# Kernel tuning notes

Hardware: AMD Instinct MI355X
Metric: run time of the kernel (lower is better)

Reference implementation:

```python
import jax, jax.numpy as jnp
import numpy as np

H = 4    # heads
DK = 5   # d_k = d_model // h = 20 // 4
D = 20   # d_model


def _proj(x, W, b):
    # x: [B,S,D] -> [B,H,S,DK]
    B, S, _ = x.shape
    y = x @ W.T + b
    return y.reshape(B, S, H, DK).transpose(0, 2, 1, 3)


def _attn(q, k, v, mask4):
    # q,k,v: [B,H,S,DK]; mask4: [B,1,1,S]
    scores = jnp.einsum('bhqd,bhkd->bhqk', q, k) / jnp.sqrt(jnp.asarray(DK, q.dtype))
    scores = jnp.where(mask4 == 0, jnp.asarray(-1e9, q.dtype), scores)
    p = jax.nn.softmax(scores, axis=-1)  # dropout omitted (eval mode)
    return jnp.einsum('bhqk,bhkd->bhqd', p, v)


def setup_inputs() -> dict:
    key = jax.random.key(0)
    ks = jax.random.split(key, 12)
    B, S = 8, 2048
    scale = 1.0 / np.sqrt(D)
    inp = {
        'query': jax.random.normal(ks[0], (B, S, D), dtype=jnp.float32),
        'key': jax.random.normal(ks[1], (B, S, D), dtype=jnp.float32),
        'value': jax.random.normal(ks[2], (B, S, D), dtype=jnp.float32),
        'mask': jax.random.randint(ks[3], (B, S), 0, 2, dtype=jnp.int32),
    }
    for i in range(4):
        inp[f'W{i}'] = jax.random.normal(ks[4 + 2 * i], (D, D), dtype=jnp.float32) * scale
        inp[f'b{i}'] = jax.random.normal(ks[5 + 2 * i], (D,), dtype=jnp.float32) * 0.01
    return inp


def reference(query, key, value, mask, W0, b0, W1, b1, W2, b2, W3, b3):
    B, S, _ = query.shape
    mask4 = mask[:, None, None, :]  # [B,1,1,S]
    # Six permuted (arg-to-linear0, arg-to-linear1, arg-to-linear2) variants,
    # exactly as the torch forward: (q,k,k),(k,q,q),(q,v,v),(v,q,q),(k,v,v),(v,k,k)
    triples = [
        (query, key, key), (key, query, query),
        (query, value, value), (value, query, query),
        (key, value, value), (value, key, key),
    ]
    out = None
    for a, bb, c in triples:
        o = _attn(_proj(a, W0, b0), _proj(bb, W1, b1), _proj(c, W2, b2), mask4)
        out = o if out is None else out + o
    # merge heads: [B,H,S,DK] -> [B,S,D]
    out = out.transpose(0, 2, 1, 3).reshape(B, S, H * DK)
    return out @ W3.T + b3
```

## Files before the change

kernel.cpp:

```cpp
#include <hip/hip_runtime.h>
#include <cstdint>
#include <cstddef>

#define B    8
#define SEQ  2048
#define H    4
#define DKN  5
#define DIM  20
#define PRE8 8
#define SENTB ((short)0xC2FC)
#define ONEB  ((short)0x3F80)
#define B128  ((short)0x4300)
#define PBIASM 12599162.0f

typedef short short8 __attribute__((ext_vector_type(8)));
typedef float f32x16 __attribute__((ext_vector_type(16)));

static __device__ __forceinline__ unsigned short bf16b(float x) {
    union { float f; unsigned u; } v; v.f = x;
    unsigned r = v.u + 0x7FFFu + ((v.u >> 16) & 1u);
    return (unsigned short)(r >> 16);
}
static __device__ __forceinline__ float bf16f(unsigned short h) {
    union { unsigned u; float f; } v; v.u = ((unsigned)h) << 16;
    return v.f;
}
static __device__ __forceinline__ unsigned pk_pbits(float ta, float tb) {
    unsigned ia, ib;
    __builtin_memcpy(&ia, &ta, 4);
    __builtin_memcpy(&ib, &tb, 4);
    return __builtin_amdgcn_perm(ib, ia, 0x05040100u);
}
static __device__ __forceinline__ int sig32(int t) {
    return (t & 19) | ((t & 4) << 1) | ((t & 8) >> 1);
}


__global__ __launch_bounds__(256) void proj_kernel(
    const float* __restrict__ q, const float* __restrict__ k, const float* __restrict__ v,
    const float* __restrict__ W0, const float* __restrict__ b0,
    const float* __restrict__ W1, const float* __restrict__ b1,
    const float* __restrict__ W2, const float* __restrict__ b2,
    const int* __restrict__ mask,
    short* __restrict__ Qt, short* __restrict__ Kt, short* __restrict__ Vt,
    int* __restrict__ meta)
{
    __shared__ float Ws[3][DIM * DIM];
    __shared__ float bsh[3][DIM];
    __shared__ int   widx[256];
    __shared__ int   cntS;

    int tid = threadIdx.x;
    int blk = blockIdx.x;
    int w   = blk & 7;  blk >>= 3;
    int h   = blk & 3;  blk >>= 2;
    int bb  = blk & 7;  blk >>= 3;
    int x   = blk;
    int s0  = w * 256;

    for (int i = tid; i < DIM * DIM; i += 256) {
        Ws[0][i] = W0[i]; Ws[1][i] = W1[i]; Ws[2][i] = W2[i];
    }
    if (tid < DIM) { bsh[0][tid] = b0[tid]; bsh[1][tid] = b1[tid]; bsh[2][tid] = b2[tid]; }

    if (tid < 64) {
        const int* mrow = mask + bb * SEQ;
        int base = 0;
        for (int ch = 0; ch < SEQ; ch += 64) {
            int mv = mrow[ch + tid];
            unsigned long long bal = __ballot(mv != 0);
            int pos = base + (int)__popcll(bal & ((1ull << tid) - 1ull));
            if (mv && pos >= s0 && pos < s0 + 256) widx[pos - s0] = ch + tid;
            base += (int)__popcll(bal);
        }
        if (tid == 0) {
            cntS = base;
            if (x == 0 && h == 0 && w == 0) meta[bb] = base;
        }
    }
    __syncthreads();

    int  cnt   = cntS;
    int  c     = s0 + tid;
    bool valid = c < cnt;
    int  gs    = valid ? widx[tid] : 0;

    const float QSC = 0.44721359549995793f * 1.4426950408889634f * 128.0f;
    const float* base = (x == 0) ? q : ((x == 1) ? k : v);

    float xq[DIM], xg[DIM];
    {
        const float4* r4 = (const float4*)(base + (size_t)(bb * SEQ + c) * DIM);
        const float4* g4 = (const float4*)(base + (size_t)(bb * SEQ + gs) * DIM);
        #pragma unroll
        for (int i = 0; i < 5; ++i) {
            float4 a = r4[i], g = g4[i];
            xq[i*4+0]=a.x; xq[i*4+1]=a.y; xq[i*4+2]=a.z; xq[i*4+3]=a.w;
            xg[i*4+0]=g.x; xg[i*4+1]=g.y; xg[i*4+2]=g.z; xg[i*4+3]=g.w;
        }
    }

    #define DOT20(xv, t, j, dst) {                                        \
        float acc_ = bsh[t][j];                                           \
        const float4* wr_ = (const float4*)&Ws[t][(j) * DIM];             \
        _Pragma("unroll")                                                 \
        for (int i4 = 0; i4 < 5; ++i4) {                                  \
            float4 w_ = wr_[i4];                                          \
            acc_ += (xv)[i4*4+0]*w_.x + (xv)[i4*4+1]*w_.y                 \
                  + (xv)[i4*4+2]*w_.z + (xv)[i4*4+3]*w_.w;                \
        }                                                                 \
        dst = acc_;                                                       \
    }

    size_t row = ((size_t)(x * B + bb) * H + h) * SEQ + c;

    short8 qhi = {0, 0, 0, 0, 0, B128, 0, 0};
    short8 qlo = {0, 0, 0, 0, 0, 0, 0, 0};
    #pragma unroll
    for (int d = 0; d < DKN; ++d) {
        float y; DOT20(xq, 0, h * DKN + d, y);
        y *= QSC;
        unsigned short hb = bf16b(y);
        qhi[d] = (short)hb;
        qlo[d] = (short)bf16b(y - bf16f(hb));
    }
    ((short8*)Qt)[row * 2 + 0] = qhi;
    ((short8*)Qt)[row * 2 + 1] = qlo;

    short8 rk = {0, 0, 0, 0, 0, valid ? (short)0 : SENTB, 0, 0};
    if (valid) {
        #pragma unroll
        for (int d = 0; d < DKN; ++d) {
            float y; DOT20(xg, 1, h * DKN + d, y);
            rk[d] = (short)bf16b(y);
        }
    }
    ((short8*)Kt)[row] = rk;

    if (valid) {
        size_t vb = ((size_t)(x * B + bb) * H + h) * 8 * SEQ;
        size_t vcell = vb + (size_t)(c >> 5) * 256 + sig32(c & 31);
        #pragma unroll
        for (int d = 0; d < DKN; ++d) {
            float y; DOT20(xg, 2, h * DKN + d, y);
            Vt[vcell + (size_t)d * 32] = (short)bf16b(y);
        }
        Vt[vcell + (size_t)5 * 32] = ONEB;
    }
}

__global__ __launch_bounds__(128, 4) void attn_kernel(
    const short* __restrict__ Qt, const short* __restrict__ Kt,
    const short* __restrict__ Vt, const int* __restrict__ meta,
    float* __restrict__ pre)
{
    int lane = threadIdx.x & 63;
    int l31  = lane & 31, half = lane >> 5;

    int wid  = blockIdx.x;
    int qtq  = wid / 192;
    int grp  = wid - qtq * 192;
    int h    = grp & 3;  grp >>= 2;
    int b    = grp & 7;  grp >>= 3;
    int p    = grp;
    int a    = (0x212010 >> (4 * p)) & 0xF;
    int kv   = (0x120201 >> (4 * p)) & 0xF;
    int qt0  = qtq * 4 + (threadIdx.x >> 6) * 2;

    int cnt  = meta[b];
    int kend = (cnt + 63) & ~63;

    const short*  Qb = Qt + ((size_t)(a  * B + b) * H + h) * SEQ * 16;
    const short8* Kb = (const short8*)Kt + ((size_t)(kv * B + b) * H + h) * SEQ;
    const short*  Vb = Vt + ((size_t)(kv * B + b) * H + h) * 8 * SEQ;
    const short*  Vr = Vb + (size_t)(l31 & 7) * 32 + half * 8;

    short8 qf[2];
    f32x16 acc[2];
    f32x16 zc = {0.f,0.f,0.f,0.f,0.f,0.f,0.f,0.f,0.f,0.f,0.f,0.f,0.f,0.f,0.f,0.f};
    f32x16 sb = {PBIASM,PBIASM,PBIASM,PBIASM,PBIASM,PBIASM,PBIASM,PBIASM,
                 PBIASM,PBIASM,PBIASM,PBIASM,PBIASM,PBIASM,PBIASM,PBIASM};
    #pragma unroll
    for (int t = 0; t < 2; ++t) {
        int qb = (qt0 + t) * 32;
        qf[t]  = *(const short8*)(Qb + (size_t)(qb + l31) * 16 + half * 8);
        acc[t] = zc;
    }

    short8 kfA = Kb[l31],      kfB = Kb[32 + l31];
    short8 vaA = *(const short8*)(Vr);
    short8 vcA = *(const short8*)(Vr + 16);
    short8 vaB = *(const short8*)(Vr + 256);
    short8 vcB = *(const short8*)(Vr + 272);

    for (int c0 = 0; c0 < kend; c0 += 64) {
        int c1 = c0 + 64;
        const short* Vn = Vr + (size_t)c1 * 8;

        short8 kfA_n = Kb[c1 + l31];
        short8 vaA_n = *(const short8*)(Vn);
        short8 vcA_n = *(const short8*)(Vn + 16);

        __builtin_amdgcn_s_setprio(1);
        #pragma unroll
        for (int t = 0; t < 2; ++t) {
            f32x16 dA = __builtin_amdgcn_mfma_f32_32x32x16_bf16(kfA, qf[t], sb, 0, 0, 0);
            unsigned p0[4], p1[4];
            #pragma unroll
            for (int r = 0; r < 4; ++r) {
                p0[r] = pk_pbits(dA[2 * r],     dA[2 * r + 1]);
                p1[r] = pk_pbits(dA[2 * r + 8], dA[2 * r + 9]);
            }
            short8 f0, f1;
            __builtin_memcpy(&f0, p0, 16);
            __builtin_memcpy(&f1, p1, 16);
            acc[t] = __builtin_amdgcn_mfma_f32_32x32x16_bf16(vaA, f0, acc[t], 0, 0, 0);
            acc[t] = __builtin_amdgcn_mfma_f32_32x32x16_bf16(vcA, f1, acc[t], 0, 0, 0);
        }
        __builtin_amdgcn_s_setprio(0);
        kfA = kfA_n; vaA = vaA_n; vcA = vcA_n;

        short8 kfB_n = Kb[c1 + 32 + l31];
        short8 vaB_n = *(const short8*)(Vn + 256);
        short8 vcB_n = *(const short8*)(Vn + 272);

        __builtin_amdgcn_s_setprio(1);
        #pragma unroll
        for (int t = 0; t < 2; ++t) {
            f32x16 dB = __builtin_amdgcn_mfma_f32_32x32x16_bf16(kfB, qf[t], sb, 0, 0, 0);
            unsigned p0[4], p1[4];
            #pragma unroll
            for (int r = 0; r < 4; ++r) {
                p0[r] = pk_pbits(dB[2 * r],     dB[2 * r + 1]);
                p1[r] = pk_pbits(dB[2 * r + 8], dB[2 * r + 9]);
            }
            short8 f0, f1;
            __builtin_memcpy(&f0, p0, 16);
            __builtin_memcpy(&f1, p1, 16);
            acc[t] = __builtin_amdgcn_mfma_f32_32x32x16_bf16(vaB, f0, acc[t], 0, 0, 0);
            acc[t] = __builtin_amdgcn_mfma_f32_32x32x16_bf16(vcB, f1, acc[t], 0, 0, 0);
        }
        __builtin_amdgcn_s_setprio(0);
        kfB = kfB_n; vaB = vaB_n; vcB = vcB_n;
    }

    float* base0 = pre + (((size_t)p * B + b) * H + h) * SEQ * PRE8;
    #pragma unroll
    for (int t = 0; t < 2; ++t) {
        int qb = (qt0 + t) * 32;
        float lv  = __shfl(acc[t][1], 32 + l31, 64);
        float inv = 1.0f / lv;
        float* dst = base0 + (size_t)(qb + l31) * PRE8;
        if (half == 0)
            *(float4*)dst = make_float4(acc[t][0]*inv, acc[t][1]*inv,
                                        acc[t][2]*inv, acc[t][3]*inv);
        else
            dst[4] = acc[t][0] * inv;
    }
}

__global__ __launch_bounds__(64) void final_kernel(
    const float* __restrict__ pre,
    const float* __restrict__ W3, const float* __restrict__ b3,
    float* __restrict__ out)
{
    __shared__ float Ws[DIM * DIM];
    __shared__ float bs[DIM];
    int tid = threadIdx.x;
    for (int i = tid; i < DIM * DIM; i += 64) Ws[i] = W3[i];
    if (tid < DIM) bs[tid] = b3[tid];
    __syncthreads();

    int g = blockIdx.x * 64 + tid;
    int b = g / SEQ;
    int s = g - b * SEQ;

    float x[DIM];
    #pragma unroll
    for (int i = 0; i < DIM; ++i) x[i] = 0.f;

    for (int p = 0; p < 6; ++p) {
        #pragma unroll
        for (int h = 0; h < H; ++h) {
            const float* sr = pre + (((size_t)p * B + b) * H + h) * SEQ * PRE8
                                  + (size_t)s * PRE8;
            float4 a = *(const float4*)sr;
            float  a4 = sr[4];
            x[h * DKN + 0] += a.x; x[h * DKN + 1] += a.y; x[h * DKN + 2] += a.z;
            x[h * DKN + 3] += a.w; x[h * DKN + 4] += a4;
        }
    }

    float y[DIM];
    for (int j = 0; j < DIM; ++j) {
        float acc = bs[j];
        const float4* wr = (const float4*)&Ws[j * DIM];
        #pragma unroll
        for (int i4 = 0; i4 < 5; ++i4) {
            float4 w = wr[i4];
            acc += x[i4*4+0]*w.x + x[i4*4+1]*w.y + x[i4*4+2]*w.z + x[i4*4+3]*w.w;
        }
        y[j] = acc;
    }
    float4* dst = (float4*)(out + (size_t)(b * SEQ + s) * DIM);
    #pragma unroll
    for (int j4 = 0; j4 < 5; ++j4)
        dst[j4] = make_float4(y[j4*4+0], y[j4*4+1], y[j4*4+2], y[j4*4+3]);
}

extern "C" void kernel_launch(void* const* d_in, const int* in_sizes, int n_in,
                              void* d_out, int out_size, void* d_ws, size_t ws_size,
                              hipStream_t stream) {
    const float* q    = (const float*)d_in[0];
    const float* k    = (const float*)d_in[1];
    const float* v    = (const float*)d_in[2];
    const int*   mask = (const int*)d_in[3];
    const float* W0 = (const float*)d_in[4];  const float* b0 = (const float*)d_in[5];
    const float* W1 = (const float*)d_in[6];  const float* b1 = (const float*)d_in[7];
    const float* W2 = (const float*)d_in[8];  const float* b2 = (const float*)d_in[9];
    const float* W3 = (const float*)d_in[10]; const float* b3 = (const float*)d_in[11];

    const size_t NROW = (size_t)3 * B * H * SEQ;
    short* Qt = (short*)d_ws;
    short* Kt = Qt + NROW * 16;
    short* Vt = Kt + NROW * 8;
    float* pre = (float*)(Vt + NROW * 8);
    int*   meta = (int*)(pre + (size_t)6 * B * H * SEQ * PRE8);
    float* out = (float*)d_out;

    proj_kernel<<<dim3(3 * B * H * (SEQ / 256)), dim3(256), 0, stream>>>(
        q, k, v, W0, b0, W1, b1, W2, b2, mask, Qt, Kt, Vt, meta);
    attn_kernel<<<dim3(6 * B * H * 16), dim3(128), 0, stream>>>(
        Qt, Kt, Vt, meta, pre);
    final_kernel<<<dim3(B * SEQ / 64), dim3(64), 0, stream>>>(pre, W3, b3, out);
}
```

Baseline: 144.0 us.

## Stage K/V tiles through LDS via async global_load_lds double buffering

Replaces direct register prefetch of K and V fragments from global memory with asynchronous global-to-LDS copies into a per-wave double buffer. Fragments are then read from LDS, with an explicit vmcnt wait ensuring the current buffer has landed while the next one loads. The aim is to cut VGPR pressure and make global loads wide and coalesced, at the cost of extra LDS traffic, LDS reads on the critical path and reliance on correct wait counts. There is no workgroup barrier because each wave uses its own buffer.

```diff
diff --git a/kernel.cpp b/kernel.cpp
--- a/kernel.cpp
+++ b/kernel.cpp
@@ -33,6 +33,12 @@
 }
 static __device__ __forceinline__ int sig32(int t) {
     return (t & 19) | ((t & 4) << 1) | ((t & 8) >> 1);
+}
+
+typedef unsigned __attribute__((address_space(1))) gas_u32;
+typedef unsigned __attribute__((address_space(3))) las_u32;
+static __device__ __forceinline__ void glds16(const void* g, void* l) {
+    __builtin_amdgcn_global_load_lds((const gas_u32*)g, (las_u32*)l, 16, 0, 0);
 }
 
 
@@ -154,6 +160,9 @@
     const short* __restrict__ Vt, const int* __restrict__ meta,
     float* __restrict__ pre)
 {
+    __shared__ char lds[2][2][2048];
+
+    int wv   = threadIdx.x >> 6;
     int lane = threadIdx.x & 63;
     int l31  = lane & 31, half = lane >> 5;
 
@@ -165,15 +174,18 @@
     int p    = grp;
     int a    = (0x212010 >> (4 * p)) & 0xF;
     int kv   = (0x120201 >> (4 * p)) & 0xF;
-    int qt0  = qtq * 4 + (threadIdx.x >> 6) * 2;
+    int qt0  = qtq * 4 + wv * 2;
 
     int cnt  = meta[b];
     int kend = (cnt + 63) & ~63;
 
-    const short*  Qb = Qt + ((size_t)(a  * B + b) * H + h) * SEQ * 16;
-    const short8* Kb = (const short8*)Kt + ((size_t)(kv * B + b) * H + h) * SEQ;
-    const short*  Vb = Vt + ((size_t)(kv * B + b) * H + h) * 8 * SEQ;
-    const short*  Vr = Vb + (size_t)(l31 & 7) * 32 + half * 8;
+    const short* Qb  = Qt + ((size_t)(a  * B + b) * H + h) * SEQ * 16;
+    const char*  Kst = (const char*)(Kt + ((size_t)(kv * B + b) * H + h) * SEQ * 8);
+    const char*  Vst = (const char*)(Vt + ((size_t)(kv * B + b) * H + h) * 8 * SEQ);
+
+    char* myl = &lds[wv][0][0];
+    int koff = l31 * 16;
+    int voff = 1024 + (l31 & 7) * 64 + half * 16;
 
     short8 qf[2];
     f32x16 acc[2];
@@ -187,61 +199,60 @@
         acc[t] = zc;
     }
 
-    short8 kfA = Kb[l31],      kfB = Kb[32 + l31];
-    short8 vaA = *(const short8*)(Vr);
-    short8 vcA = *(const short8*)(Vr + 16);
-    short8 vaB = *(const short8*)(Vr + 256);
-    short8 vcB = *(const short8*)(Vr + 272);
-
+    glds16(Kst + lane * 16, myl);
+    glds16(Vst + lane * 16, myl + 1024);
+
+    #define PVSTEP(D, VA, VC, ACC) {                                          \
+        unsigned p0_[4], p1_[4];                                              \
+        _Pragma("unroll")                                                     \
+        for (int r = 0; r < 4; ++r) {                                         \
+            p0_[r] = pk_pbits(D[2 * r],     D[2 * r + 1]);                    \
+            p1_[r] = pk_pbits(D[2 * r + 8], D[2 * r + 9]);                    \
+        }                                                                     \
+        short8 f0_, f1_;                                                      \
+        __builtin_memcpy(&f0_, p0_, 16);                                      \
+        __builtin_memcpy(&f1_, p1_, 16);                                      \
+        ACC = __builtin_amdgcn_mfma_f32_32x32x16_bf16(VA, f0_, ACC, 0, 0, 0); \
+        ACC = __builtin_amdgcn_mfma_f32_32x32x16_bf16(VC, f1_, ACC, 0, 0, 0); \
+    }
+
+    int buf = 0;
     for (int c0 = 0; c0 < kend; c0 += 64) {
-        int c1 = c0 + 64;
-        const short* Vn = Vr + (size_t)c1 * 8;
-
-        short8 kfA_n = Kb[c1 + l31];
-        short8 vaA_n = *(const short8*)(Vn);
-        short8 vcA_n = *(const short8*)(Vn + 16);
+        size_t c1b = (size_t)(c0 + 64) * 16;
+        char* nb = myl + ((buf ^ 1) << 11);
+        glds16(Kst + c1b + lane * 16, nb);
+        glds16(Vst + c1b + lane * 16, nb + 1024);
+
+        __builtin_amdgcn_sched_barrier(0);
+        asm volatile("s_waitcnt vmcnt(2)" ::: "memory");
+        __builtin_amdgcn_sched_barrier(0);
+
+        const char* cb = myl + (buf << 11);
+        short8 kfA = *(const short8*)(cb + koff);
+        short8 vaA = *(const short8*)(cb + voff);
+        short8 vcA = *(const short8*)(cb + voff + 32);
 
         __builtin_amdgcn_s_setprio(1);
         #pragma unroll
         for (int t = 0; t < 2; ++t) {
             f32x16 dA = __builtin_amdgcn_mfma_f32_32x32x16_bf16(kfA, qf[t], sb, 0, 0, 0);
-            unsigned p0[4], p1[4];
-            #pragma unroll
-            for (int r = 0; r < 4; ++r) {
-                p0[r] = pk_pbits(dA[2 * r],     dA[2 * r + 1]);
-                p1[r] = pk_pbits(dA[2 * r + 8], dA[2 * r + 9]);
-            }
-            short8 f0, f1;
-            __builtin_memcpy(&f0, p0, 16);
-            __builtin_memcpy(&f1, p1, 16);
-            acc[t] = __builtin_amdgcn_mfma_f32_32x32x16_bf16(vaA, f0, acc[t], 0, 0, 0);
-            acc[t] = __builtin_amdgcn_mfma_f32_32x32x16_bf16(vcA, f1, acc[t], 0, 0, 0);
+            PVSTEP(dA, vaA, vcA, acc[t]);
         }
         __builtin_amdgcn_s_setprio(0);
-        kfA = kfA_n; vaA = vaA_n; vcA = vcA_n;
-
-        short8 kfB_n = Kb[c1 + 32 + l31];
-        short8 vaB_n = *(const short8*)(Vn + 256);
-        short8 vcB_n = *(const short8*)(Vn + 272);
+
+        short8 kfB = *(const short8*)(cb + koff + 512);
+        short8 vaB = *(const short8*)(cb + voff + 512);
+        short8 vcB = *(const short8*)(cb + voff + 544);
 
         __builtin_amdgcn_s_setprio(1);
         #pragma unroll
         for (int t = 0; t < 2; ++t) {
             f32x16 dB = __builtin_amdgcn_mfma_f32_32x32x16_bf16(kfB, qf[t], sb, 0, 0, 0);
-            unsigned p0[4], p1[4];
-            #pragma unroll
-            for (int r = 0; r < 4; ++r) {
-                p0[r] = pk_pbits(dB[2 * r],     dB[2 * r + 1]);
-                p1[r] = pk_pbits(dB[2 * r + 8], dB[2 * r + 9]);
-            }
-            short8 f0, f1;
-            __builtin_memcpy(&f0, p0, 16);
-            __builtin_memcpy(&f1, p1, 16);
-            acc[t] = __builtin_amdgcn_mfma_f32_32x32x16_bf16(vaB, f0, acc[t], 0, 0, 0);
-            acc[t] = __builtin_amdgcn_mfma_f32_32x32x16_bf16(vcB, f1, acc[t], 0, 0, 0);
+            PVSTEP(dB, vaB, vcB, acc[t]);
         }
         __builtin_amdgcn_s_setprio(0);
-        kfB = kfB_n; vaB = vaB_n; vcB = vcB_n;
+
+        buf ^= 1;
     }
 
     float* base0 = pre + (((size_t)p * B + b) * H + h) * SEQ * PRE8;
```

Measured after the change: 137.2 us. -4.7%, faster.
